# Kernel tuning notes

Measured on AMD Instinct MI355X. Metric: run time of the kernel, lower is better.

Reference implementation:

```python
import jax, jax.numpy as jnp
import numpy as np

D_MODEL = 1024
N_HEADS = 16
HEAD_DIM = D_MODEL // N_HEADS


def setup_inputs() -> dict:
    key = jax.random.key(0)
    ks = jax.random.split(key, 5)
    T, B = 2048, 2
    x = jax.random.normal(ks[0], (T, B, D_MODEL), dtype=jnp.float32)
    s = 1.0 / np.sqrt(D_MODEL)
    Wq = jax.random.normal(ks[1], (D_MODEL, D_MODEL), dtype=jnp.float32) * s
    Wk = jax.random.normal(ks[2], (D_MODEL, D_MODEL), dtype=jnp.float32) * s
    Wv = jax.random.normal(ks[3], (D_MODEL, D_MODEL), dtype=jnp.float32) * s
    Wo = jax.random.normal(ks[4], (D_MODEL, D_MODEL), dtype=jnp.float32) * s
    return {"x": x, "Wq": Wq, "Wk": Wk, "Wv": Wv, "Wo": Wo}


def reference(x, Wq, Wk, Wv, Wo):
    T, B, C = x.shape
    H, D = N_HEADS, HEAD_DIM

    def split_heads(t):
        # (T,B,C) -> (B,H,T,D), matching view+permute(1,2,0,3)
        return t.reshape(T, B, H, D).transpose(1, 2, 0, 3)

    q = split_heads(x @ Wq.T)
    k = split_heads(x @ Wk.T)
    v = split_heads(x @ Wv.T)

    scale = 1.0 / jnp.sqrt(jnp.asarray(D, dtype=x.dtype))
    scores = jnp.einsum('bhqd,bhkd->bhqk', q, k) * scale  # (B,H,T,T)
    causal = jnp.tril(jnp.ones((T, T), dtype=bool))
    scores = jnp.where(causal, scores, jnp.asarray(-jnp.inf, dtype=scores.dtype))
    probs = jax.nn.softmax(scores, axis=-1)
    ctx = jnp.einsum('bhqk,bhkd->bhqd', probs, v)  # (B,H,T,D)
    ctx = ctx.transpose(2, 0, 1, 3).reshape(T, B, C)
    return ctx @ Wo.T
```

## Files before the change

kernel.cpp:

```cpp
#include <hip/hip_runtime.h>
#include <hip/hip_bf16.h>

#define TT 2048
#define BB 2
#define CC 1024
#define HH 16
#define DD 64
#define MM (TT * BB)

typedef short bf16x8 __attribute__((ext_vector_type(8)));
typedef float f32x4  __attribute__((ext_vector_type(4)));

__device__ inline ushort f2b(float f) {
    union { float f; unsigned u; } v; v.f = f;
    unsigned r = v.u + 0x7FFFu + ((v.u >> 16) & 1u);
    return (ushort)(r >> 16);
}

__device__ inline unsigned pack_bf16(float a, float b) {
    __hip_bfloat162 h = __float22bfloat162_rn(make_float2(a, b));
    union { __hip_bfloat162 h; unsigned u; } c; c.h = h;
    return c.u;
}

__device__ inline void gload_lds16(const ushort* g, ushort* l) {
    __builtin_amdgcn_global_load_lds(
        (const __attribute__((address_space(1))) void*)g,
        (__attribute__((address_space(3))) void*)l, 16, 0, 0);
}

#define XQUADS (MM * CC / 4)
#define WQUADS (CC * CC / 4)
__global__ __launch_bounds__(256) void conv_all(const float* __restrict__ x,
                                                const float* __restrict__ Wq,
                                                const float* __restrict__ Wk,
                                                const float* __restrict__ Wv,
                                                const float* __restrict__ Wo,
                                                ushort* __restrict__ dst) {
    int idx = blockIdx.x * 256 + threadIdx.x;
    const float* src;
    int off;
    if (idx < XQUADS) {
        src = x; off = idx;
    } else {
        int wi = (idx - XQUADS) >> 18;
        off = (idx - XQUADS) & (WQUADS - 1);
        src = (wi == 0) ? Wq : (wi == 1) ? Wk : (wi == 2) ? Wv : Wo;
    }
    float4 v = ((const float4*)src)[off];
    ushort4 o = {f2b(v.x), f2b(v.y), f2b(v.z), f2b(v.w)};
    ((ushort4*)dst)[idx] = o;
}

__global__ __launch_bounds__(256) void gemm_qkv(const ushort* __restrict__ A,
                                                const ushort* __restrict__ B0,
                                                const ushort* __restrict__ B1,
                                                const ushort* __restrict__ B2,
                                                ushort* __restrict__ Oq,
                                                ushort* __restrict__ Ok,
                                                ushort* __restrict__ Ov) {
    __shared__ __align__(16) ushort As[128 * 32];
    __shared__ __align__(16) ushort Bs[128 * 32];

    const int tid = threadIdx.x;
    const int wave = tid >> 6, lane = tid & 63;
    const int quad = lane >> 4, l16 = lane & 15;
    const int wm = wave >> 1, wn = wave & 1;

    const int bm = blockIdx.x * 128;
    const int by = blockIdx.y;
    const int wsel = by >> 3;
    const ushort* Bp = (wsel == 0) ? B0 : (wsel == 1) ? B1 : B2;
    const int bn = (by & 7) * 128;

    const int srow = lane >> 2;
    const int scol = (lane & 3) * 8;

    f32x4 acc[4][4];
#pragma unroll
    for (int i = 0; i < 4; i++)
#pragma unroll
        for (int j = 0; j < 4; j++) acc[i][j] = (f32x4){0.f, 0.f, 0.f, 0.f};

    for (int k0 = 0; k0 < CC; k0 += 32) {
#pragma unroll
        for (int i = 0; i < 2; i++) {
            const int rbase = wave * 32 + i * 16;
            gload_lds16(A + (size_t)(bm + rbase + srow) * CC + k0 + scol,
                        As + rbase * 32);
            gload_lds16(Bp + (size_t)(bn + rbase + srow) * CC + k0 + scol,
                        Bs + rbase * 32);
        }
        __syncthreads();

        bf16x8 af[4], bf[4];
#pragma unroll
        for (int mi = 0; mi < 4; mi++)
            af[mi] = *(const bf16x8*)(As + (wm * 64 + mi * 16 + l16) * 32 + quad * 8);
#pragma unroll
        for (int ni = 0; ni < 4; ni++)
            bf[ni] = *(const bf16x8*)(Bs + (wn * 64 + ni * 16 + l16) * 32 + quad * 8);
#pragma unroll
        for (int mi = 0; mi < 4; mi++)
#pragma unroll
            for (int ni = 0; ni < 4; ni++)
                acc[mi][ni] = __builtin_amdgcn_mfma_f32_16x16x32_bf16(
                    af[mi], bf[ni], acc[mi][ni], 0, 0, 0);
        __syncthreads();
    }

#pragma unroll
    for (int mi = 0; mi < 4; mi++) {
#pragma unroll
        for (int r = 0; r < 4; r++) {
            const int m = bm + wm * 64 + mi * 16 + quad * 4 + r;
#pragma unroll
            for (int ni = 0; ni < 4; ni++) {
                const int colg = bn + wn * 64 + ni * 16 + l16;
                float v = acc[mi][ni][r];
                if (wsel == 0) v *= 0.18033688f;
                const int t = m >> 1, b = m & 1;
                const int h = colg >> 6, d = colg & 63;
                ushort* dst = (wsel == 0) ? Oq : (wsel == 1) ? Ok : Ov;
                dst[(((size_t)(b * HH + h)) * TT + t) * DD + d] = f2b(v);
            }
        }
    }
}

__global__ __launch_bounds__(256) void gemm_out(const ushort* __restrict__ A,
                                                const ushort* __restrict__ Bm,
                                                float* __restrict__ Of) {
    __shared__ __align__(16) ushort As[128 * 32];
    __shared__ __align__(16) ushort Bs[64 * 32];

    const int tid = threadIdx.x;
    const int wave = tid >> 6, lane = tid & 63;
    const int quad = lane >> 4, l16 = lane & 15;

    const int bm = blockIdx.x * 128;
    const int bn = blockIdx.y * 64;

    const int srow = lane >> 2;
    const int scol = (lane & 3) * 8;

    f32x4 acc[2][4];
#pragma unroll
    for (int i = 0; i < 2; i++)
#pragma unroll
        for (int j = 0; j < 4; j++) acc[i][j] = (f32x4){0.f, 0.f, 0.f, 0.f};

    for (int k0 = 0; k0 < CC; k0 += 32) {
#pragma unroll
        for (int i = 0; i < 2; i++) {
            const int rbase = wave * 32 + i * 16;
            gload_lds16(A + (size_t)(bm + rbase + srow) * CC + k0 + scol,
                        As + rbase * 32);
        }
        gload_lds16(Bm + (size_t)(bn + wave * 16 + srow) * CC + k0 + scol,
                    Bs + wave * 16 * 32);
        __syncthreads();

        bf16x8 af[2], bf[4];
#pragma unroll
        for (int mi = 0; mi < 2; mi++)
            af[mi] = *(const bf16x8*)(As + (wave * 32 + mi * 16 + l16) * 32 + quad * 8);
#pragma unroll
        for (int ni = 0; ni < 4; ni++)
            bf[ni] = *(const bf16x8*)(Bs + (ni * 16 + l16) * 32 + quad * 8);
#pragma unroll
        for (int mi = 0; mi < 2; mi++)
#pragma unroll
            for (int ni = 0; ni < 4; ni++)
                acc[mi][ni] = __builtin_amdgcn_mfma_f32_16x16x32_bf16(
                    af[mi], bf[ni], acc[mi][ni], 0, 0, 0);
        __syncthreads();
    }

#pragma unroll
    for (int mi = 0; mi < 2; mi++)
#pragma unroll
        for (int r = 0; r < 4; r++) {
            const int m = bm + wave * 32 + mi * 16 + quad * 4 + r;
#pragma unroll
            for (int ni = 0; ni < 4; ni++)
                Of[(size_t)m * CC + bn + ni * 16 + l16] = acc[mi][ni][r];
        }
}

__global__ __launch_bounds__(256) void prep_kv(const ushort* __restrict__ Kb,
                                               const ushort* __restrict__ Vb,
                                               ushort* __restrict__ Kf,
                                               ushort* __restrict__ Vf) {
    __shared__ __align__(16) ushort Ls[64 * 72];
    const int tile = blockIdx.x;
    const int bh   = blockIdx.y;
    const int t    = threadIdx.x;
    const size_t src = (size_t)bh * TT * DD + (size_t)tile * 64 * DD;
    const size_t dst = (size_t)bh * TT * DD + (size_t)tile * 4096;

#pragma unroll
    for (int i = 0; i < 2; i++) {
        int e = t + i * 256;
        int r = e >> 3, kc = (e & 7) * 8;
        *(uint4*)(Ls + r * 72 + kc) = *(const uint4*)(Kb + src + r * 64 + kc);
    }
    __syncthreads();
#pragma unroll
    for (int i = 0; i < 2; i++) {
        int o = t + i * 256;
        int c = o >> 8, nb = (o >> 6) & 3, lane = o & 63;
        int quad = lane >> 4, l16 = lane & 15;
        int j = nb * 16 + l16, k0 = c * 32 + quad * 8;
        *(uint4*)(Kf + dst + (size_t)o * 8) = *(const uint4*)(Ls + j * 72 + k0);
    }
    __syncthreads();

#pragma unroll
    for (int i = 0; i < 2; i++) {
        int e = t + i * 256;
        int r = e >> 3, kc = (e & 7) * 8;
        *(uint4*)(Ls + r * 72 + kc) = *(const uint4*)(Vb + src + r * 64 + kc);
    }
    __syncthreads();
#pragma unroll
    for (int i = 0; i < 2; i++) {
        int o = t + i * 256;
        int c = o >> 8, db = (o >> 6) & 3, lane = o & 63;
        int quad = lane >> 4, l16 = lane & 15;
        int d = db * 16 + l16;
        ushort tmp[8];
#pragma unroll
        for (int u = 0; u < 8; u++) {
            int j = 16 * ((8 * c + u) >> 2) + 4 * quad + (u & 3);
            tmp[u] = Ls[j * 72 + d];
        }
        *(uint4*)(Vf + dst + (size_t)o * 8) = *(uint4*)tmp;
    }
}

template <bool DIAG>
__device__ __forceinline__ void attn_step(const bf16x8* qa, f32x4* O, float& l,
                                          const bf16x8* kf, const bf16x8* vf,
                                          int j0, int qg, int quad) {
    f32x4 S[4];
#pragma unroll
    for (int nb = 0; nb < 4; nb++) S[nb] = (f32x4){0.f, 0.f, 0.f, 0.f};
#pragma unroll
    for (int c = 0; c < 2; c++)
#pragma unroll
        for (int nb = 0; nb < 4; nb++)
            S[nb] = __builtin_amdgcn_mfma_f32_16x16x32_bf16(kf[c * 4 + nb],
                                                            qa[c], S[nb], 0, 0, 0);

    float p[4][4];
#pragma unroll
    for (int nb = 0; nb < 4; nb++)
#pragma unroll
        for (int r = 0; r < 4; r++) {
            float s = S[nb][r];
            if (DIAG) { if (j0 + nb * 16 + quad * 4 + r > qg) s = -1e30f; }
            p[nb][r] = __builtin_amdgcn_exp2f(s);
        }
#pragma unroll
    for (int nb = 0; nb < 4; nb++)
        l += (p[nb][0] + p[nb][1]) + (p[nb][2] + p[nb][3]);

    union { unsigned w[4]; bf16x8 v; } pa0, pa1;
#pragma unroll
    for (int w = 0; w < 4; w++) {
        const int nb = w >> 1;
        const int rb = (w & 1) * 2;
        pa0.w[w] = pack_bf16(p[nb][rb], p[nb][rb + 1]);
        pa1.w[w] = pack_bf16(p[2 + nb][rb], p[2 + nb][rb + 1]);
    }
#pragma unroll
    for (int db = 0; db < 4; db++)
        O[db] = __builtin_amdgcn_mfma_f32_16x16x32_bf16(pa0.v, vf[db], O[db], 0, 0, 0);
#pragma unroll
    for (int db = 0; db < 4; db++)
        O[db] = __builtin_amdgcn_mfma_f32_16x16x32_bf16(pa1.v, vf[4 + db], O[db], 0, 0, 0);
}

__global__ __launch_bounds__(256, 2) void attn_mfma(const ushort* __restrict__ Qb,
                                                    const ushort* __restrict__ Kf,
                                                    const ushort* __restrict__ Vf,
                                                    ushort* __restrict__ ctx) {
    __shared__ __align__(16) ushort KV[2][8192];

    const int tid  = threadIdx.x;
    const int wave = tid >> 6;
    const int lane = tid & 63;
    const int quad = lane >> 4;
    const int l16  = lane & 15;

    const int bidx = blockIdx.x;
    const int xcd  = bidx & 7;
    const int slot = bidx >> 3;
    const int bh   = xcd * 4 + (slot >> 4);
    const int p    = slot & 15;

    const int qtA = p, qtB = (TT / 64 - 1) - p;
    const int q0A = qtA * 64 + wave * 16;
    const int q0B = qtB * 64 + wave * 16;
    const int qgA = q0A + l16;
    const int qgB = q0B + l16;

    const size_t baseQK = (size_t)bh * TT * DD;

    bf16x8 qaA[2], qaB[2];
    {
        const ushort* qp = Qb + baseQK + (size_t)(q0A + l16) * DD + quad * 8;
        qaA[0] = *(const bf16x8*)(qp);
        qaA[1] = *(const bf16x8*)(qp + 32);
        const ushort* qp2 = Qb + baseQK + (size_t)(q0B + l16) * DD + quad * 8;
        qaB[0] = *(const bf16x8*)(qp2);
        qaB[1] = *(const bf16x8*)(qp2 + 32);
    }

    f32x4 OA[4], OB[4];
#pragma unroll
    for (int i = 0; i < 4; i++) {
        OA[i] = (f32x4){0.f, 0.f, 0.f, 0.f};
        OB[i] = (f32x4){0.f, 0.f, 0.f, 0.f};
    }
    float lA = 0.f, lB = 0.f;

    const ushort* Kfp = Kf + baseQK;
    const ushort* Vfp = Vf + baseQK;

    auto stage = [&](int buf, const ushort* kp, const ushort* vp) {
#pragma unroll
        for (int i = 0; i < 2; i++) {
            const int ch = wave * 2 + i;
            gload_lds16(kp + (ch << 9) + lane * 8, &KV[buf][ch << 9]);
            gload_lds16(vp + (ch << 9) + lane * 8, &KV[buf][(8 + ch) << 9]);
        }
    };

    stage(0, Kfp, Vfp);
    __syncthreads();

    int cur = 0;
    for (int kt = 0; kt <= qtB; kt++) {
        if (kt < qtB) stage(cur ^ 1, Kfp + 4096, Vfp + 4096);

        bf16x8 kf[8], vf[8];
#pragma unroll
        for (int i = 0; i < 8; i++) {
            kf[i] = *(const bf16x8*)(&KV[cur][i << 9] + lane * 8);
            vf[i] = *(const bf16x8*)(&KV[cur][(8 + i) << 9] + lane * 8);
        }

        const int j0 = kt * 64;
        if (kt == qtB)
            attn_step<true >(qaB, OB, lB, kf, vf, j0, qgB, quad);
        else
            attn_step<false>(qaB, OB, lB, kf, vf, j0, qgB, quad);

        if (kt < qtA)
            attn_step<false>(qaA, OA, lA, kf, vf, j0, qgA, quad);
        else if (kt == qtA)
            attn_step<true >(qaA, OA, lA, kf, vf, j0, qgA, quad);

        __syncthreads();
        cur ^= 1;
        Kfp += 4096;
        Vfp += 4096;
    }

    lA += __shfl_xor(lA, 16); lA += __shfl_xor(lA, 32);
    lB += __shfl_xor(lB, 16); lB += __shfl_xor(lB, 32);

    const int b = bh >> 4, h = bh & 15;
#pragma unroll
    for (int r = 0; r < 4; r++) {
        const float invA = 1.f / __shfl(lA, quad * 4 + r);
        const float invB = 1.f / __shfl(lB, quad * 4 + r);
        const int tA = q0A + quad * 4 + r;
        const int tB = q0B + quad * 4 + r;
#pragma unroll
        for (int db = 0; db < 4; db++) {
            ctx[((size_t)tA * BB + b) * CC + h * DD + db * 16 + l16] =
                f2b(OA[db][r] * invA);
            ctx[((size_t)tB * BB + b) * CC + h * DD + db * 16 + l16] =
                f2b(OB[db][r] * invB);
        }
    }
}

extern "C" void kernel_launch(void* const* d_in, const int* in_sizes, int n_in,
                              void* d_out, int out_size, void* d_ws, size_t ws_size,
                              hipStream_t stream) {
    const float* x  = (const float*)d_in[0];
    const float* Wq = (const float*)d_in[1];
    const float* Wk = (const float*)d_in[2];
    const float* Wv = (const float*)d_in[3];
    const float* Wo = (const float*)d_in[4];
    float* out = (float*)d_out;

    ushort* xb  = (ushort*)d_ws;
    ushort* Wb  = xb + (size_t)MM * CC;
    ushort* Wqb = Wb;
    ushort* Wkb = Wb + (size_t)CC * CC;
    ushort* Wvb = Wb + 2 * (size_t)CC * CC;
    ushort* Wob = Wb + 3 * (size_t)CC * CC;
    ushort* Qb  = Wb + 4 * (size_t)CC * CC;
    ushort* Kb  = Qb + (size_t)MM * CC;
    ushort* Vb  = Kb + (size_t)MM * CC;
    ushort* Kf  = Vb + (size_t)MM * CC;
    ushort* Vf  = Kf + (size_t)MM * CC;
    ushort* Ctxb = Vf + (size_t)MM * CC;

    conv_all<<<dim3((XQUADS + 4 * WQUADS) / 256), 256, 0, stream>>>(
        x, Wq, Wk, Wv, Wo, xb);

    gemm_qkv<<<dim3(MM / 128, 24), 256, 0, stream>>>(
        xb, Wqb, Wkb, Wvb, Qb, Kb, Vb);

    prep_kv<<<dim3(TT / 64, BB * HH), 256, 0, stream>>>(Kb, Vb, Kf, Vf);

    attn_mfma<<<dim3(512), 256, 0, stream>>>(Qb, Kf, Vf, Ctxb);

    gemm_out<<<dim3(MM / 128, CC / 64), 256, 0, stream>>>(Ctxb, Wob, out);
}
```

Before: 170.7 us.

## Double attention query tile to 128 rows per block, halving grid

```diff
diff --git a/kernel.cpp b/kernel.cpp
--- a/kernel.cpp
+++ b/kernel.cpp
@@ -240,49 +240,57 @@
 }
 
 template <bool DIAG>
-__device__ __forceinline__ void attn_step(const bf16x8* qa, f32x4* O, float& l,
-                                          const bf16x8* kf, const bf16x8* vf,
-                                          int j0, int qg, int quad) {
-    f32x4 S[4];
-#pragma unroll
-    for (int nb = 0; nb < 4; nb++) S[nb] = (f32x4){0.f, 0.f, 0.f, 0.f};
-#pragma unroll
-    for (int c = 0; c < 2; c++)
+__device__ __forceinline__ void attn_step64(const bf16x8* qa,
+                                            f32x4* O,
+                                            float* l,
+                                            const bf16x8* kf, const bf16x8* vf,
+                                            int j0, int qg0, int quad) {
+#pragma unroll
+    for (int m = 0; m < 2; m++) {
+        f32x4 S[4];
+#pragma unroll
+        for (int nb = 0; nb < 4; nb++) S[nb] = (f32x4){0.f, 0.f, 0.f, 0.f};
+#pragma unroll
+        for (int c = 0; c < 2; c++)
+#pragma unroll
+            for (int nb = 0; nb < 4; nb++)
+                S[nb] = __builtin_amdgcn_mfma_f32_16x16x32_bf16(
+                    kf[c * 4 + nb], qa[m * 2 + c], S[nb], 0, 0, 0);
+
+        const int qg = qg0 + m * 16;
+        float p[4][4];
 #pragma unroll
         for (int nb = 0; nb < 4; nb++)
-            S[nb] = __builtin_amdgcn_mfma_f32_16x16x32_bf16(kf[c * 4 + nb],
-                                                            qa[c], S[nb], 0, 0, 0);
-
-    float p[4][4];
-#pragma unroll
-    for (int nb = 0; nb < 4; nb++)
-#pragma unroll
-        for (int r = 0; r < 4; r++) {
-            float s = S[nb][r];
-            if (DIAG) { if (j0 + nb * 16 + quad * 4 + r > qg) s = -1e30f; }
-            p[nb][r] = __builtin_amdgcn_exp2f(s);
-        }
-#pragma unroll
-    for (int nb = 0; nb < 4; nb++)
-        l += (p[nb][0] + p[nb][1]) + (p[nb][2] + p[nb][3]);
-
-    union { unsigned w[4]; bf16x8 v; } pa0, pa1;
-#pragma unroll
-    for (int w = 0; w < 4; w++) {
-        const int nb = w >> 1;
-        const int rb = (w & 1) * 2;
-        pa0.w[w] = pack_bf16(p[nb][rb], p[nb][rb + 1]);
-        pa1.w[w] = pack_bf16(p[2 + nb][rb], p[2 + nb][rb + 1]);
-    }
-#pragma unroll
-    for (int db = 0; db < 4; db++)
-        O[db] = __builtin_amdgcn_mfma_f32_16x16x32_bf16(pa0.v, vf[db], O[db], 0, 0, 0);
-#pragma unroll
-    for (int db = 0; db < 4; db++)
-        O[db] = __builtin_amdgcn_mfma_f32_16x16x32_bf16(pa1.v, vf[4 + db], O[db], 0, 0, 0);
-}
-
-__global__ __launch_bounds__(256, 2) void attn_mfma(const ushort* __restrict__ Qb,
+#pragma unroll
+            for (int r = 0; r < 4; r++) {
+                float s = S[nb][r];
+                if (DIAG) { if (j0 + nb * 16 + quad * 4 + r > qg) s = -1e30f; }
+                p[nb][r] = __builtin_amdgcn_exp2f(s);
+            }
+#pragma unroll
+        for (int nb = 0; nb < 4; nb++)
+            l[m] += (p[nb][0] + p[nb][1]) + (p[nb][2] + p[nb][3]);
+
+        union { unsigned w[4]; bf16x8 v; } pa0, pa1;
+#pragma unroll
+        for (int w = 0; w < 4; w++) {
+            const int nb = w >> 1;
+            const int rb = (w & 1) * 2;
+            pa0.w[w] = pack_bf16(p[nb][rb], p[nb][rb + 1]);
+            pa1.w[w] = pack_bf16(p[2 + nb][rb], p[2 + nb][rb + 1]);
+        }
+#pragma unroll
+        for (int db = 0; db < 4; db++)
+            O[m * 4 + db] = __builtin_amdgcn_mfma_f32_16x16x32_bf16(
+                pa0.v, vf[db], O[m * 4 + db], 0, 0, 0);
+#pragma unroll
+        for (int db = 0; db < 4; db++)
+            O[m * 4 + db] = __builtin_amdgcn_mfma_f32_16x16x32_bf16(
+                pa1.v, vf[4 + db], O[m * 4 + db], 0, 0, 0);
+    }
+}
+
+__global__ __launch_bounds__(256, 1) void attn_mfma(const ushort* __restrict__ Qb,
                                                     const ushort* __restrict__ Kf,
                                                     const ushort* __restrict__ Vf,
                                                     ushort* __restrict__ ctx) {
@@ -297,34 +305,39 @@
     const int bidx = blockIdx.x;
     const int xcd  = bidx & 7;
     const int slot = bidx >> 3;
-    const int bh   = xcd * 4 + (slot >> 4);
-    const int p    = slot & 15;
-
-    const int qtA = p, qtB = (TT / 64 - 1) - p;
-    const int q0A = qtA * 64 + wave * 16;
-    const int q0B = qtB * 64 + wave * 16;
+    const int bh   = xcd * 4 + (slot >> 3);
+    const int p    = slot & 7;
+
+    const int qtA = p, qtB = 15 - p;
+    const int q0A = qtA * 128 + wave * 32;
+    const int q0B = qtB * 128 + wave * 32;
     const int qgA = q0A + l16;
     const int qgB = q0B + l16;
 
     const size_t baseQK = (size_t)bh * TT * DD;
 
-    bf16x8 qaA[2], qaB[2];
-    {
-        const ushort* qp = Qb + baseQK + (size_t)(q0A + l16) * DD + quad * 8;
-        qaA[0] = *(const bf16x8*)(qp);
-        qaA[1] = *(const bf16x8*)(qp + 32);
-        const ushort* qp2 = Qb + baseQK + (size_t)(q0B + l16) * DD + quad * 8;
-        qaB[0] = *(const bf16x8*)(qp2);
-        qaB[1] = *(const bf16x8*)(qp2 + 32);
-    }
-
-    f32x4 OA[4], OB[4];
-#pragma unroll
-    for (int i = 0; i < 4; i++) {
+    bf16x8 qaA[4], qaB[4];
+#pragma unroll
+    for (int m = 0; m < 2; m++) {
+        const ushort* qp = Qb + baseQK + (size_t)(q0A + m * 16 + l16) * DD + quad * 8;
+        qaA[m * 2 + 0] = *(const bf16x8*)(qp);
+        qaA[m * 2 + 1] = *(const bf16x8*)(qp + 32);
+        const ushort* qp2 = Qb + baseQK + (size_t)(q0B + m * 16 + l16) * DD + quad * 8;
+        qaB[m * 2 + 0] = *(const bf16x8*)(qp2);
+        qaB[m * 2 + 1] = *(const bf16x8*)(qp2 + 32);
+    }
+
+    f32x4 OA[8], OB[8];
+#pragma unroll
+    for (int i = 0; i < 8; i++) {
         OA[i] = (f32x4){0.f, 0.f, 0.f, 0.f};
         OB[i] = (f32x4){0.f, 0.f, 0.f, 0.f};
     }
-    float lA = 0.f, lB = 0.f;
+    float lA[2] = {0.f, 0.f}, lB[2] = {0.f, 0.f};
+
+    const int dA = 2 * qtA + (wave >> 1);
+    const int dB = 2 * qtB + (wave >> 1);
+    const int ktmax = 2 * qtB + 1;
 
     const ushort* Kfp = Kf + baseQK;
     const ushort* Vfp = Vf + baseQK;
@@ -342,8 +355,8 @@
     __syncthreads();
 
     int cur = 0;
-    for (int kt = 0; kt <= qtB; kt++) {
-        if (kt < qtB) stage(cur ^ 1, Kfp + 4096, Vfp + 4096);
+    for (int kt = 0; kt <= ktmax; kt++) {
+        if (kt < ktmax) stage(cur ^ 1, Kfp + 4096, Vfp + 4096);
 
         bf16x8 kf[8], vf[8];
 #pragma unroll
@@ -353,15 +366,15 @@
         }
 
         const int j0 = kt * 64;
-        if (kt == qtB)
-            attn_step<true >(qaB, OB, lB, kf, vf, j0, qgB, quad);
-        else
-            attn_step<false>(qaB, OB, lB, kf, vf, j0, qgB, quad);
-
-        if (kt < qtA)
-            attn_step<false>(qaA, OA, lA, kf, vf, j0, qgA, quad);
-        else if (kt == qtA)
-            attn_step<true >(qaA, OA, lA, kf, vf, j0, qgA, quad);
+        if (kt < dB)
+            attn_step64<false>(qaB, OB, lB, kf, vf, j0, qgB, quad);
+        else if (kt == dB)
+            attn_step64<true >(qaB, OB, lB, kf, vf, j0, qgB, quad);
+
+        if (kt < dA)
+            attn_step64<false>(qaA, OA, lA, kf, vf, j0, qgA, quad);
+        else if (kt == dA)
+            attn_step64<true >(qaA, OA, lA, kf, vf, j0, qgA, quad);
 
         __syncthreads();
         cur ^= 1;
@@ -369,24 +382,29 @@
         Vfp += 4096;
     }
 
-    lA += __shfl_xor(lA, 16); lA += __shfl_xor(lA, 32);
-    lB += __shfl_xor(lB, 16); lB += __shfl_xor(lB, 32);
+#pragma unroll
+    for (int m = 0; m < 2; m++) {
+        lA[m] += __shfl_xor(lA[m], 16); lA[m] += __shfl_xor(lA[m], 32);
+        lB[m] += __shfl_xor(lB[m], 16); lB[m] += __shfl_xor(lB[m], 32);
+    }
 
     const int b = bh >> 4, h = bh & 15;
 #pragma unroll
-    for (int r = 0; r < 4; r++) {
-        const float invA = 1.f / __shfl(lA, quad * 4 + r);
-        const float invB = 1.f / __shfl(lB, quad * 4 + r);
-        const int tA = q0A + quad * 4 + r;
-        const int tB = q0B + quad * 4 + r;
-#pragma unroll
-        for (int db = 0; db < 4; db++) {
-            ctx[((size_t)tA * BB + b) * CC + h * DD + db * 16 + l16] =
-                f2b(OA[db][r] * invA);
-            ctx[((size_t)tB * BB + b) * CC + h * DD + db * 16 + l16] =
-                f2b(OB[db][r] * invB);
-        }
-    }
+    for (int m = 0; m < 2; m++)
+#pragma unroll
+        for (int r = 0; r < 4; r++) {
+            const float invA = 1.f / __shfl(lA[m], quad * 4 + r);
+            const float invB = 1.f / __shfl(lB[m], quad * 4 + r);
+            const int tA = q0A + m * 16 + quad * 4 + r;
+            const int tB = q0B + m * 16 + quad * 4 + r;
+#pragma unroll
+            for (int db = 0; db < 4; db++) {
+                ctx[((size_t)tA * BB + b) * CC + h * DD + db * 16 + l16] =
+                    f2b(OA[m * 4 + db][r] * invA);
+                ctx[((size_t)tB * BB + b) * CC + h * DD + db * 16 + l16] =
+                    f2b(OB[m * 4 + db][r] * invB);
+            }
+        }
 }
 
 extern "C" void kernel_launch(void* const* d_in, const int* in_sizes, int n_in,
@@ -420,7 +438,7 @@
 
     prep_kv<<<dim3(TT / 64, BB * HH), 256, 0, stream>>>(Kb, Vb, Kf, Vf);
 
-    attn_mfma<<<dim3(512), 256, 0, stream>>>(Qb, Kf, Vf, Ctxb);
+    attn_mfma<<<dim3(256), 256, 0, stream>>>(Qb, Kf, Vf, Ctxb);
 
     gemm_out<<<dim3(MM / 128, CC / 64), 256, 0, stream>>>(Ctxb, Wob, out);
 }
```

Measured after the change: 178.1 us. 4.3% more time.
